# Kernel tuning notes

Measured on AMD Instinct MI355X. Metric: run time of the kernel, lower is better.

Reference implementation:

```python
import jax, jax.numpy as jnp
import numpy as np

ALPHA = 0.2          # LeakyReLU negative slope
NEG_INF = -9e15      # mask value used by the original pygat implementation


def gat_layer(x, adj, W, a_src, a_dst, concat):
    """Dense multi-head GAT layer (pygat-style GraphAttentionLayer).

    x: [N, F_in], adj: [N, N] bool, W: [K, F_in, H], a_src/a_dst: [K, H].
    Returns [N, K*H] (concat=True, with ELU) or [N, H] (concat=False, mean heads).
    """
    h = jnp.einsum('nf,kfh->knh', x, W)                      # [K, N, H]
    f_src = jnp.einsum('knh,kh->kn', h, a_src)               # [K, N]
    f_dst = jnp.einsum('knh,kh->kn', h, a_dst)               # [K, N]
    e = jax.nn.leaky_relu(f_src[:, :, None] + f_dst[:, None, :], ALPHA)  # [K, N, N]
    e = jnp.where(adj[None, :, :], e, NEG_INF)
    att = jax.nn.softmax(e, axis=-1)                         # masked softmax over neighbors
    out = jnp.einsum('knm,kmh->knh', att, h)                 # [K, N, H]
    if concat:
        K, N, H = out.shape
        return jax.nn.elu(jnp.transpose(out, (1, 0, 2)).reshape(N, K * H))
    return out.mean(axis=0)                                  # [N, H]


def setup_inputs() -> dict:
    key = jax.random.key(0)
    ks = jax.random.split(key, 8)
    N, Fdim, H, K, C = 8192, 512, 128, 2, 16
    x = jax.random.normal(ks[0], (N, Fdim), dtype=jnp.float32)
    # sparse-ish binary adjacency, avg degree ~32, with self loops
    adj = jax.random.uniform(ks[1], (N, N)) < (32.0 / N)
    adj = adj | jnp.eye(N, dtype=bool)
    s1 = 1.0 / np.sqrt(Fdim)
    s2 = 1.0 / np.sqrt(K * H)
    W1 = jax.random.normal(ks[2], (K, Fdim, H), dtype=jnp.float32) * s1
    a1_src = jax.random.normal(ks[3], (K, H), dtype=jnp.float32) * s1
    a1_dst = jax.random.normal(ks[4], (K, H), dtype=jnp.float32) * s1
    W2 = jax.random.normal(ks[5], (1, K * H, C), dtype=jnp.float32) * s2
    a2_src = jax.random.normal(ks[6], (1, C), dtype=jnp.float32) * s2
    a2_dst = jax.random.normal(ks[7], (1, C), dtype=jnp.float32) * s2
    return {"x": x, "adj": adj, "W1": W1, "a1_src": a1_src, "a1_dst": a1_dst,
            "W2": W2, "a2_src": a2_src, "a2_dst": a2_dst}


def reference(x, adj, W1, a1_src, a1_dst, W2, a2_src, a2_dst):
    h1 = gat_layer(x, adj, W1, a1_src, a1_dst, concat=True)   # [N, K*H]
    h1 = jax.nn.relu(h1)                                      # dropout p=0.0 -> identity
    out = gat_layer(h1, adj, W2, a2_src, a2_dst, concat=False)  # [N, C]
    return out
```

## Files before the change

### kernel.cpp

```cpp
#include <hip/hip_runtime.h>
#include <hip/hip_bf16.h>
#include <math.h>

constexpr int NN   = 8192;
constexpr int FIN  = 512;
constexpr int HC   = 256;
constexpr int COUT = 16;
constexpr int MAXD = 128;

typedef __attribute__((ext_vector_type(8))) short bf16x8;
typedef __attribute__((ext_vector_type(4))) float f32x4;

__device__ __forceinline__ float lrelu(float x) { return x > 0.f ? x : 0.2f * x; }

__device__ __forceinline__ unsigned short f2bf(float f) {
  unsigned u = __float_as_uint(f);
  return (unsigned short)((u + 0x7fffu + ((u >> 16) & 1u)) >> 16);
}
__device__ __forceinline__ float bf2f(unsigned short h) {
  unsigned u = ((unsigned)h) << 16;
  return __uint_as_float(u);
}

__global__ __launch_bounds__(256) void prep_kernel(const float* __restrict__ x,
                                                   const float* __restrict__ W1,
                                                   unsigned short* __restrict__ Xh,
                                                   unsigned short* __restrict__ Xl,
                                                   unsigned short* __restrict__ Wth,
                                                   unsigned short* __restrict__ Wtl,
                                                   float* __restrict__ fs,
                                                   float* __restrict__ fd) {
  int b = blockIdx.x;
  if (b < 4096) {
    int t = b * 256 + threadIdx.x;
    float4 v = *reinterpret_cast<const float4*>(x + (size_t)t * 4);
    ushort4 hi, lo;
    hi.x = f2bf(v.x); lo.x = f2bf(v.x - bf2f(hi.x));
    hi.y = f2bf(v.y); lo.y = f2bf(v.y - bf2f(hi.y));
    hi.z = f2bf(v.z); lo.z = f2bf(v.z - bf2f(hi.z));
    hi.w = f2bf(v.w); lo.w = f2bf(v.w - bf2f(hi.w));
    *reinterpret_cast<ushort4*>(Xh + (size_t)t * 4) = hi;
    *reinterpret_cast<ushort4*>(Xl + (size_t)t * 4) = lo;
  } else if (b < 4608) {
    int idx = (b - 4096) * 256 + threadIdx.x;
    int n = idx >> 9, kk = idx & 511;
    int k = n >> 7, h = n & 127;
    float v = W1[k * 65536 + kk * 128 + h];
    unsigned short hi = f2bf(v);
    Wth[idx] = hi;
    Wtl[idx] = f2bf(v - bf2f(hi));
  } else {
    int z = (b - 4608) * 256 + threadIdx.x;
    if (z < 2 * NN) fs[z] = 0.f;
    else fd[z - 2 * NN] = 0.f;
  }
}

__global__ __launch_bounds__(256) void gemm1m(const unsigned short* __restrict__ Xh,
                                              const unsigned short* __restrict__ Xl,
                                              const unsigned short* __restrict__ Bh,
                                              const unsigned short* __restrict__ Bl,
                                              const float* __restrict__ a1s,
                                              const float* __restrict__ a1d,
                                              float* __restrict__ Hout,
                                              float* __restrict__ fs,
                                              float* __restrict__ fd) {
  int wave = threadIdx.x >> 6, lane = threadIdx.x & 63;
  int rowBase = blockIdx.x * 128 + wave * 32;
  int colBase = blockIdx.y * 64;
  int frow = lane & 15;
  int kchunk = (lane >> 4) * 8;
  f32x4 acc[2][4] = {};
  for (int k0 = 0; k0 < FIN; k0 += 32) {
    bf16x8 ah[2], al[2], bh[4], bl[4];
#pragma unroll
    for (int r = 0; r < 2; ++r) {
      size_t off = (size_t)(rowBase + r * 16 + frow) * FIN + k0 + kchunk;
      ah[r] = *reinterpret_cast<const bf16x8*>(Xh + off);
      al[r] = *reinterpret_cast<const bf16x8*>(Xl + off);
    }
#pragma unroll
    for (int c = 0; c < 4; ++c) {
      size_t off = (size_t)(colBase + c * 16 + frow) * FIN + k0 + kchunk;
      bh[c] = *reinterpret_cast<const bf16x8*>(Bh + off);
      bl[c] = *reinterpret_cast<const bf16x8*>(Bl + off);
    }
#pragma unroll
    for (int r = 0; r < 2; ++r)
#pragma unroll
      for (int c = 0; c < 4; ++c) {
        acc[r][c] = __builtin_amdgcn_mfma_f32_16x16x32_bf16(ah[r], bh[c], acc[r][c], 0, 0, 0);
        acc[r][c] = __builtin_amdgcn_mfma_f32_16x16x32_bf16(ah[r], bl[c], acc[r][c], 0, 0, 0);
        acc[r][c] = __builtin_amdgcn_mfma_f32_16x16x32_bf16(al[r], bh[c], acc[r][c], 0, 0, 0);
      }
  }
  int dcol = lane & 15, drow4 = (lane >> 4) * 4;
#pragma unroll
  for (int r = 0; r < 2; ++r)
#pragma unroll
    for (int c = 0; c < 4; ++c)
#pragma unroll
      for (int q = 0; q < 4; ++q)
        Hout[(size_t)(rowBase + r * 16 + drow4 + q) * HC + colBase + c * 16 + dcol] =
            acc[r][c][q];
  int khead = colBase >> 7;
  float as[4], ad[4];
#pragma unroll
  for (int c = 0; c < 4; ++c) {
    as[c] = a1s[colBase + c * 16 + dcol];
    ad[c] = a1d[colBase + c * 16 + dcol];
  }
#pragma unroll
  for (int r = 0; r < 2; ++r)
#pragma unroll
    for (int q = 0; q < 4; ++q) {
      float s = 0.f, d = 0.f;
#pragma unroll
      for (int c = 0; c < 4; ++c) {
        float v = acc[r][c][q];
        s += v * as[c];
        d += v * ad[c];
      }
#pragma unroll
      for (int off = 8; off > 0; off >>= 1) {
        s += __shfl_xor(s, off, 16);
        d += __shfl_xor(d, off, 16);
      }
      if ((lane & 15) == 0) {
        int row = rowBase + r * 16 + drow4 + q;
        atomicAdd(fs + khead * NN + row, s);
        atomicAdd(fd + khead * NN + row, d);
      }
    }
}

__global__ __launch_bounds__(256) void attn1_kernel(const void* __restrict__ adj,
                                                    int* __restrict__ nbr,
                                                    int* __restrict__ cnt,
                                                    const float* __restrict__ H,
                                                    const float* __restrict__ fs,
                                                    const float* __restrict__ fd,
                                                    float* __restrict__ H1) {
  __shared__ float att[2][MAXD];
  __shared__ int jidx[MAXD];
  __shared__ int scnt;
  __shared__ int sflag;
  int i = blockIdx.x;
  int t = threadIdx.x;
  if (t == 0) scnt = 0;
  if (t < 64) {
    size_t idx = (size_t)(t * 32) * (size_t)(NN + 1);
    int v = ((const int*)adj)[idx];
    bool four = (v == 1) || (v == 0x3f800000);
    unsigned long long b = __ballot(four);
    if (t == 0) sflag = (b == ~0ull) ? 1 : 0;
  }
  __syncthreads();
  if (sflag) {
    const int4* row = reinterpret_cast<const int4*>((const int*)adj + (size_t)i * NN);
#pragma unroll
    for (int rep = 0; rep < 8; ++rep) {
      int vi = rep * 256 + t;
      int4 v = row[vi];
      int base = vi * 4;
      if (v.x) { int p = atomicAdd(&scnt, 1); if (p < MAXD) jidx[p] = base; }
      if (v.y) { int p = atomicAdd(&scnt, 1); if (p < MAXD) jidx[p] = base + 1; }
      if (v.z) { int p = atomicAdd(&scnt, 1); if (p < MAXD) jidx[p] = base + 2; }
      if (v.w) { int p = atomicAdd(&scnt, 1); if (p < MAXD) jidx[p] = base + 3; }
    }
  } else {
    const uint4* row = reinterpret_cast<const uint4*>((const unsigned char*)adj + (size_t)i * NN);
#pragma unroll
    for (int rep = 0; rep < 2; ++rep) {
      int vi = rep * 256 + t;
      uint4 v = row[vi];
      int base = vi * 16;
      unsigned w[4] = {v.x, v.y, v.z, v.w};
#pragma unroll
      for (int q = 0; q < 4; ++q)
#pragma unroll
        for (int bb = 0; bb < 4; ++bb)
          if ((w[q] >> (8 * bb)) & 0xffu) {
            int p = atomicAdd(&scnt, 1);
            if (p < MAXD) jidx[p] = base + q * 4 + bb;
          }
    }
  }
  __syncthreads();
  int deg = scnt < MAXD ? scnt : MAXD;
  if (t == 0) cnt[i] = deg;
  if (t < deg) {
    int j = jidx[t];
    nbr[(size_t)i * MAXD + t] = j;
    att[0][t] = lrelu(fs[i] + fd[j]);
    att[1][t] = lrelu(fs[NN + i] + fd[NN + j]);
  }
  __syncthreads();
  int wave = t >> 6, lane = t & 63;
  if (wave < 2) {
    int k = wave;
    float e0 = (lane < deg) ? att[k][lane] : -INFINITY;
    float e1 = (lane + 64 < deg) ? att[k][lane + 64] : -INFINITY;
    float m = fmaxf(e0, e1);
#pragma unroll
    for (int off = 32; off > 0; off >>= 1) m = fmaxf(m, __shfl_xor(m, off));
    float p0 = (lane < deg) ? expf(e0 - m) : 0.f;
    float p1 = (lane + 64 < deg) ? expf(e1 - m) : 0.f;
    float s = p0 + p1;
#pragma unroll
    for (int off = 32; off > 0; off >>= 1) s += __shfl_xor(s, off);
    float inv = 1.f / s;
    if (lane < deg) att[k][lane] = p0 * inv;
    if (lane + 64 < deg) att[k][lane + 64] = p1 * inv;
  }
  __syncthreads();
  int k = t >> 7;
  float acc = 0.f;
  int q = 0;
  for (; q + 4 <= deg; q += 4) {
    float a0 = att[k][q], a1 = att[k][q + 1], a2 = att[k][q + 2], a3 = att[k][q + 3];
    int j0 = jidx[q], j1 = jidx[q + 1], j2 = jidx[q + 2], j3 = jidx[q + 3];
    float g0 = H[(size_t)j0 * HC + t];
    float g1 = H[(size_t)j1 * HC + t];
    float g2 = H[(size_t)j2 * HC + t];
    float g3 = H[(size_t)j3 * HC + t];
    acc += a0 * g0 + a1 * g1 + a2 * g2 + a3 * g3;
  }
  for (; q < deg; ++q) acc += att[k][q] * H[(size_t)jidx[q] * HC + t];
  H1[(size_t)i * HC + t] = fmaxf(acc, 0.f);
}

__global__ __launch_bounds__(256) void gemm2_kernel(const float* __restrict__ H1,
                                                    const float* __restrict__ W2,
                                                    const float* __restrict__ a2s,
                                                    const float* __restrict__ a2d,
                                                    float* __restrict__ H2,
                                                    float* __restrict__ f2s,
                                                    float* __restrict__ f2d) {
  __shared__ float Ws[HC * COUT];
  int tid = threadIdx.x;
#pragma unroll
  for (int r = 0; r < 16; ++r) Ws[r * 256 + tid] = W2[r * 256 + tid];
  __syncthreads();
  int rg = tid >> 4, c = tid & 15;
  int n = blockIdx.x * 16 + rg;
  const float* h1r = H1 + (size_t)n * HC;
  float acc = 0.f;
#pragma unroll 8
  for (int kk = 0; kk < HC; ++kk) acc += h1r[kk] * Ws[kk * COUT + c];
  H2[(size_t)n * COUT + c] = acc;
  float s = acc * a2s[c];
  float d = acc * a2d[c];
#pragma unroll
  for (int off = 8; off > 0; off >>= 1) {
    s += __shfl_xor(s, off, 16);
    d += __shfl_xor(d, off, 16);
  }
  if (c == 0) { f2s[n] = s; f2d[n] = d; }
}

__global__ __launch_bounds__(64) void attn2_kernel(const int* __restrict__ nbr,
                                                   const int* __restrict__ cnt,
                                                   const float* __restrict__ H2,
                                                   const float* __restrict__ fs,
                                                   const float* __restrict__ fd,
                                                   float* __restrict__ out) {
  __shared__ float att[MAXD];
  __shared__ int jj[MAXD];
  int i = blockIdx.x;
  int lane = threadIdx.x;
  int deg = cnt[i];
  float fsi = fs[i];
  int j0 = (lane < deg) ? nbr[(size_t)i * MAXD + lane] : 0;
  int j1 = (lane + 64 < deg) ? nbr[(size_t)i * MAXD + lane + 64] : 0;
  float e0 = (lane < deg) ? lrelu(fsi + fd[j0]) : -INFINITY;
  float e1 = (lane + 64 < deg) ? lrelu(fsi + fd[j1]) : -INFINITY;
  float m = fmaxf(e0, e1);
#pragma unroll
  for (int off = 32; off > 0; off >>= 1) m = fmaxf(m, __shfl_xor(m, off));
  float p0 = (lane < deg) ? expf(e0 - m) : 0.f;
  float p1 = (lane + 64 < deg) ? expf(e1 - m) : 0.f;
  float s = p0 + p1;
#pragma unroll
  for (int off = 32; off > 0; off >>= 1) s += __shfl_xor(s, off);
  float inv = 1.f / s;
  att[lane] = p0 * inv;
  att[lane + 64] = p1 * inv;
  jj[lane] = j0;
  jj[lane + 64] = j1;
  __syncthreads();
  if (lane < COUT) {
    float acc = 0.f;
    for (int q = 0; q < deg; ++q) acc += att[q] * H2[(size_t)jj[q] * COUT + lane];
    out[(size_t)i * COUT + lane] = acc;
  }
}

extern "C" void kernel_launch(void* const* d_in, const int* in_sizes, int n_in,
                              void* d_out, int out_size, void* d_ws, size_t ws_size,
                              hipStream_t stream) {
  const float* x   = (const float*)d_in[0];
  const void*  adj = d_in[1];
  const float* W1  = (const float*)d_in[2];
  const float* a1s = (const float*)d_in[3];
  const float* a1d = (const float*)d_in[4];
  const float* W2  = (const float*)d_in[5];
  const float* a2s = (const float*)d_in[6];
  const float* a2d = (const float*)d_in[7];
  float* out = (float*)d_out;

  char* ws = (char*)d_ws;
  size_t off = 0;
  auto alloc = [&](size_t bytes) -> void* {
    void* p = ws + off;
    off = (off + bytes + 255) & ~(size_t)255;
    return p;
  };
  int*            nbr  = (int*)           alloc((size_t)NN * MAXD * 4);
  int*            cnt  = (int*)           alloc((size_t)NN * 4);
  unsigned short* Xh   = (unsigned short*)alloc((size_t)NN * FIN * 2);
  unsigned short* Xl   = (unsigned short*)alloc((size_t)NN * FIN * 2);
  unsigned short* Wth  = (unsigned short*)alloc((size_t)HC * FIN * 2);
  unsigned short* Wtl  = (unsigned short*)alloc((size_t)HC * FIN * 2);
  float*          H    = (float*)         alloc((size_t)NN * HC * 4);
  float*          fs   = (float*)         alloc((size_t)2 * NN * 4);
  float*          fd   = (float*)         alloc((size_t)2 * NN * 4);
  float*          H1   = (float*)         alloc((size_t)NN * HC * 4);
  float*          H2   = (float*)         alloc((size_t)NN * COUT * 4);
  float*          f2s  = (float*)         alloc((size_t)NN * 4);
  float*          f2d  = (float*)         alloc((size_t)NN * 4);

  hipLaunchKernelGGL(prep_kernel, dim3(4736), dim3(256), 0, stream,
                     x, W1, Xh, Xl, Wth, Wtl, fs, fd);
  hipLaunchKernelGGL(gemm1m, dim3(NN / 128, HC / 64), dim3(256), 0, stream,
                     Xh, Xl, Wth, Wtl, a1s, a1d, H, fs, fd);
  hipLaunchKernelGGL(attn1_kernel, dim3(NN), dim3(256), 0, stream,
                     adj, nbr, cnt, H, fs, fd, H1);
  hipLaunchKernelGGL(gemm2_kernel, dim3(NN / 16), dim3(256), 0, stream,
                     H1, W2, a2s, a2d, H2, f2s, f2d);
  hipLaunchKernelGGL(attn2_kernel, dim3(NN), dim3(64), 0, stream,
                     nbr, cnt, H2, f2s, f2d, out);
}
```

Measured before the change: 438.7 us.

## Fuse layer-2 projection and attention logits into attn1 epilogue

Removes gemm2_kernel and instead computes H2 = relu(H1)·W2 in the tail of attn1_kernel. Each thread multiplies its H1 element by a register-held row of W2, then reduces across each wave with shuffles and across waves through shared memory. The f2s/f2d logits are produced in the same kernel. This drops the H1 global buffer write and read and one kernel launch, at the cost of 16 wave-wide shuffle reductions, an extra barrier and 16 more registers per attn1 block.

```diff
diff --git a/kernel.cpp b/kernel.cpp
--- a/kernel.cpp
+++ b/kernel.cpp
@@ -140,13 +140,22 @@
                                                     const float* __restrict__ H,
                                                     const float* __restrict__ fs,
                                                     const float* __restrict__ fd,
-                                                    float* __restrict__ H1) {
+                                                    const float* __restrict__ W2,
+                                                    const float* __restrict__ a2s,
+                                                    const float* __restrict__ a2d,
+                                                    float* __restrict__ H2,
+                                                    float* __restrict__ f2s,
+                                                    float* __restrict__ f2d) {
   __shared__ float att[2][MAXD];
   __shared__ int jidx[MAXD];
   __shared__ int scnt;
   __shared__ int sflag;
+  __shared__ float wred[4][COUT];
   int i = blockIdx.x;
   int t = threadIdx.x;
+  float w2r[COUT];
+#pragma unroll
+  for (int c = 0; c < COUT; ++c) w2r[c] = W2[t * COUT + c];
   if (t == 0) scnt = 0;
   if (t < 64) {
     size_t idx = (size_t)(t * 32) * (size_t)(NN + 1);
@@ -227,36 +236,33 @@
     acc += a0 * g0 + a1 * g1 + a2 * g2 + a3 * g3;
   }
   for (; q < deg; ++q) acc += att[k][q] * H[(size_t)jidx[q] * HC + t];
-  H1[(size_t)i * HC + t] = fmaxf(acc, 0.f);
-}
-
-__global__ __launch_bounds__(256) void gemm2_kernel(const float* __restrict__ H1,
-                                                    const float* __restrict__ W2,
-                                                    const float* __restrict__ a2s,
-                                                    const float* __restrict__ a2d,
-                                                    float* __restrict__ H2,
-                                                    float* __restrict__ f2s,
-                                                    float* __restrict__ f2d) {
-  __shared__ float Ws[HC * COUT];
-  int tid = threadIdx.x;
-#pragma unroll
-  for (int r = 0; r < 16; ++r) Ws[r * 256 + tid] = W2[r * 256 + tid];
-  __syncthreads();
-  int rg = tid >> 4, c = tid & 15;
-  int n = blockIdx.x * 16 + rg;
-  const float* h1r = H1 + (size_t)n * HC;
-  float acc = 0.f;
-#pragma unroll 8
-  for (int kk = 0; kk < HC; ++kk) acc += h1r[kk] * Ws[kk * COUT + c];
-  H2[(size_t)n * COUT + c] = acc;
-  float s = acc * a2s[c];
-  float d = acc * a2d[c];
-#pragma unroll
-  for (int off = 8; off > 0; off >>= 1) {
-    s += __shfl_xor(s, off, 16);
-    d += __shfl_xor(d, off, 16);
-  }
-  if (c == 0) { f2s[n] = s; f2d[n] = d; }
+  float h1 = fmaxf(acc, 0.f);
+
+  float p[COUT];
+#pragma unroll
+  for (int c = 0; c < COUT; ++c) {
+    float v = h1 * w2r[c];
+#pragma unroll
+    for (int off = 32; off > 0; off >>= 1) v += __shfl_xor(v, off);
+    p[c] = v;
+  }
+  if (lane == 0) {
+#pragma unroll
+    for (int c = 0; c < COUT; ++c) wred[wave][c] = p[c];
+  }
+  __syncthreads();
+  if (t < COUT) {
+    float h2c = wred[0][t] + wred[1][t] + wred[2][t] + wred[3][t];
+    H2[(size_t)i * COUT + t] = h2c;
+    float s = h2c * a2s[t];
+    float d = h2c * a2d[t];
+#pragma unroll
+    for (int off = 8; off > 0; off >>= 1) {
+      s += __shfl_xor(s, off, 16);
+      d += __shfl_xor(d, off, 16);
+    }
+    if (t == 0) { f2s[i] = s; f2d[i] = d; }
+  }
 }
 
 __global__ __launch_bounds__(64) void attn2_kernel(const int* __restrict__ nbr,
@@ -325,7 +331,6 @@
   float*          H    = (float*)         alloc((size_t)NN * HC * 4);
   float*          fs   = (float*)         alloc((size_t)2 * NN * 4);
   float*          fd   = (float*)         alloc((size_t)2 * NN * 4);
-  float*          H1   = (float*)         alloc((size_t)NN * HC * 4);
   float*          H2   = (float*)         alloc((size_t)NN * COUT * 4);
   float*          f2s  = (float*)         alloc((size_t)NN * 4);
   float*          f2d  = (float*)         alloc((size_t)NN * 4);
@@ -335,9 +340,7 @@
   hipLaunchKernelGGL(gemm1m, dim3(NN / 128, HC / 64), dim3(256), 0, stream,
                      Xh, Xl, Wth, Wtl, a1s, a1d, H, fs, fd);
   hipLaunchKernelGGL(attn1_kernel, dim3(NN), dim3(256), 0, stream,
-                     adj, nbr, cnt, H, fs, fd, H1);
-  hipLaunchKernelGGL(gemm2_kernel, dim3(NN / 16), dim3(256), 0, stream,
-                     H1, W2, a2s, a2d, H2, f2s, f2d);
+                     adj, nbr, cnt, H, fs, fd, W2, a2s, a2d, H2, f2s, f2d);
   hipLaunchKernelGGL(attn2_kernel, dim3(NN), dim3(64), 0, stream,
                      nbr, cnt, H2, f2s, f2d, out);
 }
```

Measured after the change: 448.2 us. +2.2%, slower.
